# Kernel tuning notes

Hardware: AMD Instinct MI355X
Metric: run time of the kernel (lower is better)

Reference implementation:

```python
import jax, jax.numpy as jnp
import numpy as np

B, N, D_DIM = 64, 512, 1024


def setup_inputs() -> dict:
    key = jax.random.key(0)
    kd, kh, ku, kw = jax.random.split(key, 4)
    D = jax.random.normal(kd, (B, N, D_DIM), dtype=jnp.float32)
    H = jax.random.normal(kh, (B, N, D_DIM), dtype=jnp.float32)
    # learned params (torch inits to zeros; use small random for a meaningful baseline)
    U = jax.random.normal(ku, (D_DIM, D_DIM + 1), dtype=jnp.float32) * 0.02
    W = jax.random.normal(kw, (2 * D_DIM + 1,), dtype=jnp.float32) * 0.02
    return {"D": D, "H": H, "U": U, "W": W}


def reference(D, H, U, W):
    b, n, d = D.shape
    ones = jnp.ones((b, n, 1), dtype=H.dtype)
    Ha = jnp.concatenate([H, ones], axis=2)            # [B, N, d+1]
    # bilinear term: D . U . Ha^T  ->  [B, N, N]  (x indexes D, y indexes H)
    DU = jnp.einsum('bxi,ij->bxj', D, U)               # [B, N, d+1]
    U_product = jnp.einsum('bxj,byj->bxy', DU, Ha)     # [B, N, N]
    # separable linear term: W . concat(Ha[x], D[y])  (avoids [B,N,N,2d+1])
    W_h = W[: d + 1]                                   # [d+1]
    W_d = W[d + 1 :]                                   # [d]
    W_product = jnp.einsum('bxj,j->bx', Ha, W_h)[:, :, None] \
              + jnp.einsum('byi,i->by', D, W_d)[:, None, :]   # [B, N, N]
    return U_product + W_product
```

## Files before the change

### kernel.cpp

```cpp
#include <hip/hip_runtime.h>
#include <cstdint>
#include <cstddef>

typedef __bf16 bf16x8 __attribute__((ext_vector_type(8)));
typedef float f32x4 __attribute__((ext_vector_type(4)));

__device__ static inline unsigned short f32_to_bf16_rne(float f) {
  unsigned int u = __float_as_uint(f);
  unsigned int r = 0x7FFFu + ((u >> 16) & 1u);
  return (unsigned short)((u + r) >> 16);
}

__device__ static inline void async16(const void* g, void* l) {
  __builtin_amdgcn_global_load_lds(
      (const __attribute__((address_space(1))) void*)g,
      (__attribute__((address_space(3))) void*)l,
      16, 0, 0);
}

__global__ __launch_bounds__(256) void prep_Ucol(const float* __restrict__ U,
                                                 float* __restrict__ Ucol) {
  const int i = blockIdx.x * 256 + threadIdx.x;
  Ucol[i] = U[(size_t)i * 1025 + 1024];
}

__global__ __launch_bounds__(256) void prep_U(const float* __restrict__ U,
                                              unsigned short* __restrict__ Ut) {
  __shared__ float tile[32][33];
  const int i0 = blockIdx.y * 32, j0 = blockIdx.x * 32;
  const int tx = threadIdx.x & 31, ty = threadIdx.x >> 5;
#pragma unroll
  for (int r = 0; r < 32; r += 8)
    tile[ty + r][tx] = U[(size_t)(i0 + ty + r) * 1025 + j0 + tx];
  __syncthreads();
#pragma unroll
  for (int r = 0; r < 32; r += 8)
    Ut[(size_t)(j0 + ty + r) * 1024 + i0 + tx] =
        f32_to_bf16_rne(tile[tx][ty + r]);
}

__global__ __launch_bounds__(256) void prep_rows(
    const float* __restrict__ D, const float* __restrict__ H,
    const float* __restrict__ Ucol, const float* __restrict__ W,
    unsigned short* __restrict__ Db, unsigned short* __restrict__ Hb,
    float* __restrict__ cvec, float* __restrict__ tvec) {
  const int r = blockIdx.x;
  const int t = threadIdx.x;
  const size_t base = (size_t)r * 1024;
  const int i = t * 4;

  float4 d4 = *(const float4*)(D + base + i);
  float4 h4 = *(const float4*)(H + base + i);
  float4 uc = *(const float4*)(Ucol + i);
  float4 wh = *(const float4*)(W + i);
  float4 wd = *(const float4*)(W + 1025 + i);

  ushort4 db, hb;
  db.x = f32_to_bf16_rne(d4.x); db.y = f32_to_bf16_rne(d4.y);
  db.z = f32_to_bf16_rne(d4.z); db.w = f32_to_bf16_rne(d4.w);
  hb.x = f32_to_bf16_rne(h4.x); hb.y = f32_to_bf16_rne(h4.y);
  hb.z = f32_to_bf16_rne(h4.z); hb.w = f32_to_bf16_rne(h4.w);
  *(ushort4*)(Db + base + i) = db;
  *(ushort4*)(Hb + base + i) = hb;

  float cp = d4.x * uc.x + d4.y * uc.y + d4.z * uc.z + d4.w * uc.w +
             h4.x * wh.x + h4.y * wh.y + h4.z * wh.z + h4.w * wh.w;
  float tp = d4.x * wd.x + d4.y * wd.y + d4.z * wd.z + d4.w * wd.w;

#pragma unroll
  for (int off = 32; off > 0; off >>= 1) {
    cp += __shfl_down(cp, off);
    tp += __shfl_down(tp, off);
  }
  __shared__ float red[8];
  const int lane = t & 63, wv = t >> 6;
  if (lane == 0) { red[wv] = cp; red[4 + wv] = tp; }
  __syncthreads();
  if (t == 0) {
    cvec[r] = red[0] + red[1] + red[2] + red[3] + W[1024];
    tvec[r] = red[4] + red[5] + red[6] + red[7];
  }
}

template <bool FUSED>
__global__ __launch_bounds__(256) void gemm_bt(
    const unsigned short* __restrict__ A, const unsigned short* __restrict__ Bt,
    void* __restrict__ Cv, const float* __restrict__ rowBias,
    const float* __restrict__ colBias, int M, int N, int K,
    long sA, long sB, long sC) {
  __shared__ unsigned short As[128 * 64];
  __shared__ unsigned short Bs[128 * 64];

  const int tid = threadIdx.x;
  const int lane = tid & 63;
  const int wave = tid >> 6;
  const int wm = wave >> 1, wn = wave & 1;
  const int bz = blockIdx.z;
  const int m0 = blockIdx.y * 128;
  const int n0 = blockIdx.x * 128;

  const unsigned short* Ab = A + (size_t)bz * (size_t)sA;
  const unsigned short* Bb = Bt + (size_t)bz * (size_t)sB;

  size_t aOff[4], bOff[4];
  int ldsOff[4];
#pragma unroll
  for (int q = 0; q < 4; ++q) {
    int e = (q * 256 + tid) * 8;
    int row = e >> 6;
    int ch = (e >> 3) & 7;
    int chSw = ch ^ (row & 7);
    ldsOff[q] = e;
    aOff[q] = (size_t)(m0 + row) * K + chSw * 8;
    bOff[q] = (size_t)(n0 + row) * K + chSw * 8;
  }

  const f32x4 zero = {0.0f, 0.0f, 0.0f, 0.0f};
  f32x4 acc[4][4];
#pragma unroll
  for (int i = 0; i < 4; ++i)
#pragma unroll
    for (int j = 0; j < 4; ++j) acc[i][j] = zero;

  const int rr = lane & 15;
  const int qd = lane >> 4;
  const int c0 = qd ^ (rr & 7);
  const int aRow = (wm * 64 + rr) * 64;
  const int bRow = (wn * 64 + rr) * 64;

  for (int k0 = 0; k0 < K; k0 += 64) {
#pragma unroll
    for (int q = 0; q < 4; ++q) async16(Ab + aOff[q] + k0, &As[ldsOff[q]]);
#pragma unroll
    for (int q = 0; q < 4; ++q) async16(Bb + bOff[q] + k0, &Bs[ldsOff[q]]);
    __syncthreads();

#pragma unroll
    for (int kk = 0; kk < 64; kk += 32) {
      const int co = (c0 ^ (kk >> 3)) * 8;
      bf16x8 af[4], bfr[4];
#pragma unroll
      for (int mt = 0; mt < 4; ++mt)
        af[mt] = *(const bf16x8*)&As[aRow + mt * 16 * 64 + co];
#pragma unroll
      for (int nt = 0; nt < 4; ++nt)
        bfr[nt] = *(const bf16x8*)&Bs[bRow + nt * 16 * 64 + co];
#pragma unroll
      for (int mt = 0; mt < 4; ++mt)
#pragma unroll
        for (int nt = 0; nt < 4; ++nt)
          acc[mt][nt] = __builtin_amdgcn_mfma_f32_16x16x32_bf16(
              af[mt], bfr[nt], acc[mt][nt], 0, 0, 0);
    }
    __syncthreads();
  }

  const int cl = lane & 15;
  const int rq = (lane >> 4) * 4;
  if constexpr (FUSED) {
    float* Cf = (float*)Cv + (size_t)bz * (size_t)sC;
#pragma unroll
    for (int mt = 0; mt < 4; ++mt) {
      const int rbase = wm * 64 + mt * 16 + rq;
#pragma unroll
      for (int nt = 0; nt < 4; ++nt) {
        const int c = n0 + wn * 64 + nt * 16 + cl;
        const float cb = colBias[(size_t)bz * N + c];
#pragma unroll
        for (int r = 0; r < 4; ++r) {
          const int gr = m0 + rbase + r;
          Cf[(size_t)gr * N + c] =
              acc[mt][nt][r] + rowBias[(size_t)bz * M + gr] + cb;
        }
      }
    }
  } else {
    unsigned short* Cu = (unsigned short*)Cv;
#pragma unroll
    for (int mt = 0; mt < 4; ++mt) {
      const int rbase = wm * 64 + mt * 16 + rq;
#pragma unroll
      for (int nt = 0; nt < 4; ++nt) {
        const int c = n0 + wn * 64 + nt * 16 + cl;
#pragma unroll
        for (int r = 0; r < 4; ++r) {
          const int gr = m0 + rbase + r;
          Cu[(size_t)gr * N + c] = f32_to_bf16_rne(acc[mt][nt][r]);
        }
      }
    }
  }
}

extern "C" void kernel_launch(void* const* d_in, const int* in_sizes, int n_in,
                              void* d_out, int out_size, void* d_ws,
                              size_t ws_size, hipStream_t stream) {
  const float* D = (const float*)d_in[0];
  const float* H = (const float*)d_in[1];
  const float* U = (const float*)d_in[2];
  const float* W = (const float*)d_in[3];
  float* out = (float*)d_out;

  char* ws = (char*)d_ws;
  const size_t SZ = (size_t)32768 * 1024 * 2;
  unsigned short* Db = (unsigned short*)(ws);
  unsigned short* Hb = (unsigned short*)(ws + SZ);
  unsigned short* DU = (unsigned short*)(ws + 2 * SZ);
  unsigned short* Ut = (unsigned short*)(ws + 3 * SZ);
  float* cvec = (float*)(ws + 3 * SZ + (size_t)1024 * 1024 * 2);
  float* tvec = cvec + 32768;
  float* Ucol = tvec + 32768;

  prep_Ucol<<<dim3(4), dim3(256), 0, stream>>>(U, Ucol);
  prep_U<<<dim3(32, 32), dim3(256), 0, stream>>>(U, Ut);
  prep_rows<<<dim3(32768), dim3(256), 0, stream>>>(D, H, Ucol, W, Db, Hb, cvec, tvec);

  gemm_bt<false><<<dim3(8, 256, 1), dim3(256), 0, stream>>>(
      Db, Ut, (void*)DU, nullptr, nullptr, 32768, 1024, 1024, 0, 0, 0);

  gemm_bt<true><<<dim3(4, 4, 64), dim3(256), 0, stream>>>(
      DU, Hb, (void*)out, cvec, tvec, 512, 512, 1024,
      (long)512 * 1024, (long)512 * 1024, (long)512 * 512);
}
```

Baseline: 455.6 us.

## Process 16 rows per block in prep_rows and swizzle workgroups in the big GEMM

prep_rows now gives each block 16 rows, with 16 threads per row and more loads in flight per thread. It reduces with shuffles inside a 16-lane group instead of through shared memory, and launches 2048 blocks instead of 32768. The first GEMM also remaps workgroup IDs, interleaving them by groups of 8, which is meant to spread tiles across XCDs for better L2 locality on MI355X. The risks are more registers per thread in prep_rows and a different cache behaviour from the swizzle.

```diff
diff --git a/kernel.cpp b/kernel.cpp
--- a/kernel.cpp
+++ b/kernel.cpp
@@ -39,50 +39,66 @@
         f32_to_bf16_rne(tile[tx][ty + r]);
 }
 
-__global__ __launch_bounds__(256) void prep_rows(
+__global__ __launch_bounds__(256, 8) void prep_rows(
     const float* __restrict__ D, const float* __restrict__ H,
     const float* __restrict__ Ucol, const float* __restrict__ W,
     unsigned short* __restrict__ Db, unsigned short* __restrict__ Hb,
     float* __restrict__ cvec, float* __restrict__ tvec) {
-  const int r = blockIdx.x;
-  const int t = threadIdx.x;
-  const size_t base = (size_t)r * 1024;
-  const int i = t * 4;
-
-  float4 d4 = *(const float4*)(D + base + i);
-  float4 h4 = *(const float4*)(H + base + i);
-  float4 uc = *(const float4*)(Ucol + i);
-  float4 wh = *(const float4*)(W + i);
-  float4 wd = *(const float4*)(W + 1025 + i);
-
-  ushort4 db, hb;
-  db.x = f32_to_bf16_rne(d4.x); db.y = f32_to_bf16_rne(d4.y);
-  db.z = f32_to_bf16_rne(d4.z); db.w = f32_to_bf16_rne(d4.w);
-  hb.x = f32_to_bf16_rne(h4.x); hb.y = f32_to_bf16_rne(h4.y);
-  hb.z = f32_to_bf16_rne(h4.z); hb.w = f32_to_bf16_rne(h4.w);
-  *(ushort4*)(Db + base + i) = db;
-  *(ushort4*)(Hb + base + i) = hb;
-
-  float cp = d4.x * uc.x + d4.y * uc.y + d4.z * uc.z + d4.w * uc.w +
-             h4.x * wh.x + h4.y * wh.y + h4.z * wh.z + h4.w * wh.w;
-  float tp = d4.x * wd.x + d4.y * wd.y + d4.z * wd.z + d4.w * wd.w;
-
-#pragma unroll
-  for (int off = 32; off > 0; off >>= 1) {
-    cp += __shfl_down(cp, off);
-    tp += __shfl_down(tp, off);
-  }
-  __shared__ float red[8];
-  const int lane = t & 63, wv = t >> 6;
-  if (lane == 0) { red[wv] = cp; red[4 + wv] = tp; }
-  __syncthreads();
-  if (t == 0) {
-    cvec[r] = red[0] + red[1] + red[2] + red[3] + W[1024];
-    tvec[r] = red[4] + red[5] + red[6] + red[7];
-  }
-}
-
-template <bool FUSED>
+  const int tid = threadIdx.x;
+  const int rloc = tid >> 4;
+  const int seg = tid & 15;
+  const int grow = blockIdx.x * 16 + rloc;
+  const size_t base = (size_t)grow * 1024;
+
+  float cp = 0.0f, tp = 0.0f;
+#pragma unroll
+  for (int g = 0; g < 4; ++g) {
+    float4 d4[4], h4[4];
+#pragma unroll
+    for (int q = 0; q < 4; ++q) {
+      const int col = seg * 4 + (g * 4 + q) * 64;
+      d4[q] = *(const float4*)(D + base + col);
+      h4[q] = *(const float4*)(H + base + col);
+    }
+#pragma unroll
+    for (int q = 0; q < 4; ++q) {
+      const int col = seg * 4 + (g * 4 + q) * 64;
+      const float4 uc = *(const float4*)(Ucol + col);
+      const float4 wh = *(const float4*)(W + col);
+      const float4 wd = *(const float4*)(W + 1025 + col);
+
+      ushort4 db, hb;
+      db.x = f32_to_bf16_rne(d4[q].x); db.y = f32_to_bf16_rne(d4[q].y);
+      db.z = f32_to_bf16_rne(d4[q].z); db.w = f32_to_bf16_rne(d4[q].w);
+      hb.x = f32_to_bf16_rne(h4[q].x); hb.y = f32_to_bf16_rne(h4[q].y);
+      hb.z = f32_to_bf16_rne(h4[q].z); hb.w = f32_to_bf16_rne(h4[q].w);
+      *(ushort4*)(Db + base + col) = db;
+      *(ushort4*)(Hb + base + col) = hb;
+
+      cp += d4[q].x * uc.x + d4[q].y * uc.y + d4[q].z * uc.z +
+            d4[q].w * uc.w;
+      cp += h4[q].x * wh.x + h4[q].y * wh.y + h4[q].z * wh.z +
+            h4[q].w * wh.w;
+      tp += d4[q].x * wd.x + d4[q].y * wd.y + d4[q].z * wd.z +
+            d4[q].w * wd.w;
+    }
+  }
+
+  cp += __shfl_down(cp, 8);
+  tp += __shfl_down(tp, 8);
+  cp += __shfl_down(cp, 4);
+  tp += __shfl_down(tp, 4);
+  cp += __shfl_down(cp, 2);
+  tp += __shfl_down(tp, 2);
+  cp += __shfl_down(cp, 1);
+  tp += __shfl_down(tp, 1);
+  if (seg == 0) {
+    cvec[grow] = cp + W[1024];
+    tvec[grow] = tp;
+  }
+}
+
+template <bool FUSED, bool XSWZ>
 __global__ __launch_bounds__(256) void gemm_bt(
     const unsigned short* __restrict__ A, const unsigned short* __restrict__ Bt,
     void* __restrict__ Cv, const float* __restrict__ rowBias,
@@ -96,8 +112,17 @@
   const int wave = tid >> 6;
   const int wm = wave >> 1, wn = wave & 1;
   const int bz = blockIdx.z;
-  const int m0 = blockIdx.y * 128;
-  const int n0 = blockIdx.x * 128;
+
+  int bx = blockIdx.x, by = blockIdx.y;
+  if constexpr (XSWZ) {
+    const int nwg = gridDim.x * gridDim.y;
+    const int b = by * gridDim.x + bx;
+    const int s = (b & 7) * (nwg >> 3) + (b >> 3);
+    bx = s % gridDim.x;
+    by = s / gridDim.x;
+  }
+  const int m0 = by * 128;
+  const int n0 = bx * 128;
 
   const unsigned short* Ab = A + (size_t)bz * (size_t)sA;
   const unsigned short* Bb = Bt + (size_t)bz * (size_t)sB;
@@ -213,12 +238,13 @@
 
   prep_Ucol<<<dim3(4), dim3(256), 0, stream>>>(U, Ucol);
   prep_U<<<dim3(32, 32), dim3(256), 0, stream>>>(U, Ut);
-  prep_rows<<<dim3(32768), dim3(256), 0, stream>>>(D, H, Ucol, W, Db, Hb, cvec, tvec);
-
-  gemm_bt<false><<<dim3(8, 256, 1), dim3(256), 0, stream>>>(
+  prep_rows<<<dim3(2048), dim3(256), 0, stream>>>(D, H, Ucol, W, Db, Hb, cvec,
+                                                  tvec);
+
+  gemm_bt<false, true><<<dim3(8, 256, 1), dim3(256), 0, stream>>>(
       Db, Ut, (void*)DU, nullptr, nullptr, 32768, 1024, 1024, 0, 0, 0);
 
-  gemm_bt<true><<<dim3(4, 4, 64), dim3(256), 0, stream>>>(
+  gemm_bt<true, false><<<dim3(4, 4, 64), dim3(256), 0, stream>>>(
       DU, Hb, (void*)out, cvec, tvec, 512, 512, 1024,
       (long)512 * 1024, (long)512 * 1024, (long)512 * 512);
 }
```

Measured after the change: 476.1 us. 4.5% more time.

## Fuse prep kernels into one launch and swizzle block order for XCD locality

Applied to the files above, without the earlier changes.

Merges the three preprocessing kernels (U last-column gather, U transpose to bf16, row conversion and bias dot products) into a single launch, so the first 1024 blocks also perform a U transpose tile. Each thread now gathers the U last-column values with strided loads instead of reading a precomputed vector. The large DU GEMM gets a block-index remap that assigns contiguous tile ranges to each group of eight round-robin blocks, intended to improve L2 reuse across MI355X XCDs. The aim is to cut launch overhead and improve cache locality, at the cost of extra uncoalesced loads in every prep block.

```diff
diff --git a/kernel.cpp b/kernel.cpp
--- a/kernel.cpp
+++ b/kernel.cpp
@@ -18,40 +18,39 @@
       16, 0, 0);
 }
 
-__global__ __launch_bounds__(256) void prep_Ucol(const float* __restrict__ U,
-                                                 float* __restrict__ Ucol) {
-  const int i = blockIdx.x * 256 + threadIdx.x;
-  Ucol[i] = U[(size_t)i * 1025 + 1024];
-}
-
-__global__ __launch_bounds__(256) void prep_U(const float* __restrict__ U,
-                                              unsigned short* __restrict__ Ut) {
+__global__ __launch_bounds__(256) void prep_all(
+    const float* __restrict__ D, const float* __restrict__ H,
+    const float* __restrict__ U, const float* __restrict__ W,
+    unsigned short* __restrict__ Db, unsigned short* __restrict__ Hb,
+    unsigned short* __restrict__ Ut, float* __restrict__ cvec,
+    float* __restrict__ tvec) {
   __shared__ float tile[32][33];
-  const int i0 = blockIdx.y * 32, j0 = blockIdx.x * 32;
-  const int tx = threadIdx.x & 31, ty = threadIdx.x >> 5;
-#pragma unroll
-  for (int r = 0; r < 32; r += 8)
-    tile[ty + r][tx] = U[(size_t)(i0 + ty + r) * 1025 + j0 + tx];
-  __syncthreads();
-#pragma unroll
-  for (int r = 0; r < 32; r += 8)
-    Ut[(size_t)(j0 + ty + r) * 1024 + i0 + tx] =
-        f32_to_bf16_rne(tile[tx][ty + r]);
-}
-
-__global__ __launch_bounds__(256) void prep_rows(
-    const float* __restrict__ D, const float* __restrict__ H,
-    const float* __restrict__ Ucol, const float* __restrict__ W,
-    unsigned short* __restrict__ Db, unsigned short* __restrict__ Hb,
-    float* __restrict__ cvec, float* __restrict__ tvec) {
+  __shared__ float red[8];
+  const int t = threadIdx.x;
   const int r = blockIdx.x;
-  const int t = threadIdx.x;
+
+  if (r < 1024) {
+    const int i0 = (r >> 5) * 32, j0 = (r & 31) * 32;
+    const int tx = t & 31, ty = t >> 5;
+#pragma unroll
+    for (int rr = 0; rr < 32; rr += 8)
+      tile[ty + rr][tx] = U[(size_t)(i0 + ty + rr) * 1025 + j0 + tx];
+    __syncthreads();
+#pragma unroll
+    for (int rr = 0; rr < 32; rr += 8)
+      Ut[(size_t)(j0 + ty + rr) * 1024 + i0 + tx] =
+          f32_to_bf16_rne(tile[tx][ty + rr]);
+  }
+
   const size_t base = (size_t)r * 1024;
   const int i = t * 4;
 
   float4 d4 = *(const float4*)(D + base + i);
   float4 h4 = *(const float4*)(H + base + i);
-  float4 uc = *(const float4*)(Ucol + i);
+  float uc0 = U[(size_t)(i + 0) * 1025 + 1024];
+  float uc1 = U[(size_t)(i + 1) * 1025 + 1024];
+  float uc2 = U[(size_t)(i + 2) * 1025 + 1024];
+  float uc3 = U[(size_t)(i + 3) * 1025 + 1024];
   float4 wh = *(const float4*)(W + i);
   float4 wd = *(const float4*)(W + 1025 + i);
 
@@ -63,7 +62,7 @@
   *(ushort4*)(Db + base + i) = db;
   *(ushort4*)(Hb + base + i) = hb;
 
-  float cp = d4.x * uc.x + d4.y * uc.y + d4.z * uc.z + d4.w * uc.w +
+  float cp = d4.x * uc0 + d4.y * uc1 + d4.z * uc2 + d4.w * uc3 +
              h4.x * wh.x + h4.y * wh.y + h4.z * wh.z + h4.w * wh.w;
   float tp = d4.x * wd.x + d4.y * wd.y + d4.z * wd.z + d4.w * wd.w;
 
@@ -72,7 +71,6 @@
     cp += __shfl_down(cp, off);
     tp += __shfl_down(tp, off);
   }
-  __shared__ float red[8];
   const int lane = t & 63, wv = t >> 6;
   if (lane == 0) { red[wv] = cp; red[4 + wv] = tp; }
   __syncthreads();
@@ -82,7 +80,7 @@
   }
 }
 
-template <bool FUSED>
+template <bool FUSED, bool XSWZ>
 __global__ __launch_bounds__(256) void gemm_bt(
     const unsigned short* __restrict__ A, const unsigned short* __restrict__ Bt,
     void* __restrict__ Cv, const float* __restrict__ rowBias,
@@ -96,8 +94,17 @@
   const int wave = tid >> 6;
   const int wm = wave >> 1, wn = wave & 1;
   const int bz = blockIdx.z;
-  const int m0 = blockIdx.y * 128;
-  const int n0 = blockIdx.x * 128;
+
+  int bx = blockIdx.x, by = blockIdx.y;
+  if constexpr (XSWZ) {
+    const int nwg = gridDim.x * gridDim.y;
+    const int b = by * gridDim.x + bx;
+    const int s = (b & 7) * (nwg >> 3) + (b >> 3);
+    bx = s % gridDim.x;
+    by = s / gridDim.x;
+  }
+  const int m0 = by * 128;
+  const int n0 = bx * 128;
 
   const unsigned short* Ab = A + (size_t)bz * (size_t)sA;
   const unsigned short* Bb = Bt + (size_t)bz * (size_t)sB;
@@ -209,16 +216,14 @@
   unsigned short* Ut = (unsigned short*)(ws + 3 * SZ);
   float* cvec = (float*)(ws + 3 * SZ + (size_t)1024 * 1024 * 2);
   float* tvec = cvec + 32768;
-  float* Ucol = tvec + 32768;
-
-  prep_Ucol<<<dim3(4), dim3(256), 0, stream>>>(U, Ucol);
-  prep_U<<<dim3(32, 32), dim3(256), 0, stream>>>(U, Ut);
-  prep_rows<<<dim3(32768), dim3(256), 0, stream>>>(D, H, Ucol, W, Db, Hb, cvec, tvec);
-
-  gemm_bt<false><<<dim3(8, 256, 1), dim3(256), 0, stream>>>(
+
+  prep_all<<<dim3(32768), dim3(256), 0, stream>>>(D, H, U, W, Db, Hb, Ut,
+                                                  cvec, tvec);
+
+  gemm_bt<false, true><<<dim3(8, 256, 1), dim3(256), 0, stream>>>(
       Db, Ut, (void*)DU, nullptr, nullptr, 32768, 1024, 1024, 0, 0, 0);
 
-  gemm_bt<true><<<dim3(4, 4, 64), dim3(256), 0, stream>>>(
+  gemm_bt<true, false><<<dim3(4, 4, 64), dim3(256), 0, stream>>>(
       DU, Hb, (void*)out, cvec, tvec, 512, 512, 1024,
       (long)512 * 1024, (long)512 * 1024, (long)512 * 512);
 }
```

Measured after the change: 623.4 us. 36.8% more time.
